# Kernel optimization log

Hardware: AMD Instinct MI355X
Metric: run time of the kernel (lower is better)

The kernel has to match this reference:

```python
import jax, jax.numpy as jnp
import numpy as np
import math

B, S, D, H = 2, 2048, 1024, 16
DH = D // H  # dim_per_head = 64


def setup_inputs() -> dict:
    key = jax.random.key(0)
    ks = jax.random.split(key, 12)
    s = 1.0 / math.sqrt(D)
    return {
        "key": jax.random.normal(ks[0], (B, S, D), jnp.float32),
        "value": jax.random.normal(ks[1], (B, S, D), jnp.float32),
        "query": jax.random.normal(ks[2], (B, S, D), jnp.float32),
        "mask": jax.random.randint(ks[3], (B, S, S), 0, 2).astype(bool),
        "Wq": jax.random.normal(ks[4], (D, D), jnp.float32) * s,
        "bq": jnp.zeros((D,), jnp.float32),
        "Wk": jax.random.normal(ks[5], (D, D), jnp.float32) * s,
        "bk": jnp.zeros((D,), jnp.float32),
        "Wv": jax.random.normal(ks[6], (D, D), jnp.float32) * s,
        "bv": jnp.zeros((D,), jnp.float32),
        "Wo": jax.random.normal(ks[7], (D, D), jnp.float32) * s,
        "bo": jnp.zeros((D,), jnp.float32),
    }


def _shape(x):
    # [B, S, D] -> [B, H, S, DH]
    return x.reshape(B, -1, H, DH).transpose(0, 2, 1, 3)


def reference(key, value, query, mask, Wq, bq, Wk, bk, Wv, bv, Wo, bo):
    q = _shape(query @ Wq.T + bq)  # [B,H,Sq,DH]
    k = _shape(key @ Wk.T + bk)    # [B,H,Sk,DH]
    v = _shape(value @ Wv.T + bv)  # [B,H,Sk,DH]
    q = q / jnp.sqrt(jnp.asarray(DH, q.dtype))
    scores = jnp.einsum("bhqd,bhkd->bhqk", q, k)
    scores = jnp.where(mask[:, None, :, :], jnp.asarray(-1e18, scores.dtype), scores)
    attn = jax.nn.softmax(scores, axis=-1)
    # dropout is identity in eval/deterministic reference
    ctx = jnp.einsum("bhqk,bhkd->bhqd", attn, v)
    ctx = ctx.transpose(0, 2, 1, 3).reshape(B, -1, D)  # unshape
    return ctx @ Wo.T + bo
```

## Files before the change

### kernel.cpp

```cpp
#include <hip/hip_runtime.h>
#include <math.h>


constexpr int Bc  = 2;
constexpr int Sc  = 2048;
constexpr int Dc  = 1024;
constexpr int Hc  = 16;
constexpr int DHc = 64;
constexpr int BSc = Bc * Sc;

constexpr float LOG2E = 1.4426950408889634f;

typedef __bf16 bf16x8 __attribute__((ext_vector_type(8)));
typedef __bf16 bf16x4 __attribute__((ext_vector_type(4)));
typedef __bf16 bf16x2 __attribute__((ext_vector_type(2)));
typedef float  f32x4  __attribute__((ext_vector_type(4)));
typedef float  f32x16 __attribute__((ext_vector_type(16)));
typedef unsigned uint32x2 __attribute__((ext_vector_type(2)));
typedef unsigned uint32x4 __attribute__((ext_vector_type(4)));

#define GLDS16(gp, lp) __builtin_amdgcn_global_load_lds( \
    (const __attribute__((address_space(1))) void*)(gp), \
    (__attribute__((address_space(3))) void*)(lp), 16, 0, 0)

__global__ __launch_bounds__(256)
void wsplit(const float* __restrict__ W0, const float* __restrict__ W1,
            const float* __restrict__ W2, const float* __restrict__ W3,
            __bf16* __restrict__ out)
{
    const float* src[4] = {W0, W1, W2, W3};
    const int z = blockIdx.y;
    const size_t idx = ((size_t)blockIdx.x * 256 + threadIdx.x) * 4;
    const float4 v = *(const float4*)&src[z][idx];
    bf16x4 o;
    o[0] = (__bf16)v.x; o[1] = (__bf16)v.y; o[2] = (__bf16)v.z; o[3] = (__bf16)v.w;
    *(bf16x4*)&out[(size_t)z * Dc * Dc + idx] = o;
}

__global__ __launch_bounds__(256)
void acast(const float* __restrict__ A0, const float* __restrict__ A1,
           const float* __restrict__ A2, __bf16* __restrict__ out)
{
    const float* src[3] = {A0, A1, A2};
    const int z = blockIdx.y;
    const size_t idx = ((size_t)blockIdx.x * 256 + threadIdx.x) * 8;
    const float4 a = *(const float4*)&src[z][idx];
    const float4 b = *(const float4*)&src[z][idx + 4];
    bf16x8 o;
    o[0] = (__bf16)a.x; o[1] = (__bf16)a.y; o[2] = (__bf16)a.z; o[3] = (__bf16)a.w;
    o[4] = (__bf16)b.x; o[5] = (__bf16)b.y; o[6] = (__bf16)b.z; o[7] = (__bf16)b.w;
    *(bf16x8*)&out[(size_t)z * BSc * Dc + idx] = o;
}

__device__ __forceinline__ void sweep128bb(const __bf16* __restrict__ A,
                                           const __bf16* __restrict__ Wh,
                                           char* AsB, char* WsB,
                                           int gm0, int gn0, f32x4 acc[4][4])
{
    const int tid  = threadIdx.x;
    const int w    = tid >> 6;
    const int lane = tid & 63;
    const int cc   = lane & 15;
    const int g    = lane >> 4;
    const int wm   = (w & 1) * 64;
    const int wn   = (w >> 1) * 64;

    int wrow[4], wchk[4];
#pragma unroll
    for (int r = 0; r < 4; ++r) {
        const int L = r * 256 + tid;
        wrow[r] = L >> 3;
        wchk[r] = (L & 7) ^ (wrow[r] & 7);
    }

#pragma unroll
    for (int r = 0; r < 4; ++r) {
        GLDS16(Wh + (size_t)(gn0 + wrow[r]) * Dc + wchk[r] * 8,
               WsB + (r * 256 + tid) * 16);
        GLDS16(A + (size_t)(gm0 + wrow[r]) * Dc + wchk[r] * 8,
               AsB + (r * 256 + tid) * 16);
    }

    for (int it = 0; it < Dc / 64; ++it) {
        const char* As = AsB + (it & 1) * 16384;
        const char* Ws = WsB + (it & 1) * 16384;
        __syncthreads();

        if (it + 1 < Dc / 64) {
            const int kn = (it + 1) * 64;
            char* Wn = WsB + ((it + 1) & 1) * 16384;
            char* An = AsB + ((it + 1) & 1) * 16384;
#pragma unroll
            for (int r = 0; r < 4; ++r) {
                GLDS16(Wh + (size_t)(gn0 + wrow[r]) * Dc + kn + wchk[r] * 8,
                       Wn + (r * 256 + tid) * 16);
                GLDS16(A + (size_t)(gm0 + wrow[r]) * Dc + kn + wchk[r] * 8,
                       An + (r * 256 + tid) * 16);
            }
        }

        __builtin_amdgcn_s_setprio(1);
#pragma unroll
        for (int kk = 0; kk < 2; ++kk) {
            const int cb4 = (kk * 4 + g) << 4;
            bf16x8 af[4], bfr[4];
#pragma unroll
            for (int mt = 0; mt < 4; ++mt) {
                const int row = wm + mt * 16 + cc;
                af[mt] = *(const bf16x8*)(As + row * 128 + (cb4 ^ ((row & 7) << 4)));
            }
#pragma unroll
            for (int nt = 0; nt < 4; ++nt) {
                const int row = wn + nt * 16 + cc;
                bfr[nt] = *(const bf16x8*)(Ws + row * 128 + (cb4 ^ ((row & 7) << 4)));
            }
#pragma unroll
            for (int mt = 0; mt < 4; ++mt)
#pragma unroll
                for (int nt = 0; nt < 4; ++nt)
                    acc[mt][nt] = __builtin_amdgcn_mfma_f32_16x16x32_bf16(
                        af[mt], bfr[nt], acc[mt][nt], 0, 0, 0);
        }
        __builtin_amdgcn_s_setprio(0);
    }
}

__device__ __forceinline__ void sweep64p(const __bf16* __restrict__ Ahi,
                                         const __bf16* __restrict__ Alo,
                                         const __bf16* __restrict__ Wh,
                                         char* WsB, char* AhB, char* AlB,
                                         int gm0, int gn0, f32x4 acc[2][4])
{
    const int tid  = threadIdx.x;
    const int w    = tid >> 6;
    const int lane = tid & 63;
    const int cc   = lane & 15;
    const int g    = lane >> 4;
    const int wm   = (w & 1) * 32;
    const int wn   = (w >> 1) * 64;

    int wrow[4], wchk[4];
#pragma unroll
    for (int r = 0; r < 4; ++r) {
        const int L = r * 256 + tid;
        wrow[r] = L >> 3;
        wchk[r] = (L & 7) ^ (wrow[r] & 7);
    }
    int arow[2], achk[2];
#pragma unroll
    for (int r = 0; r < 2; ++r) {
        const int L = r * 256 + tid;
        arow[r] = L >> 3;
        achk[r] = (L & 7) ^ (arow[r] & 7);
    }

#pragma unroll
    for (int r = 0; r < 4; ++r)
        GLDS16(Wh + (size_t)(gn0 + wrow[r]) * Dc + wchk[r] * 8,
               WsB + (r * 256 + tid) * 16);
#pragma unroll
    for (int r = 0; r < 2; ++r) {
        GLDS16(Ahi + (size_t)(gm0 + arow[r]) * Dc + achk[r] * 8,
               AhB + (r * 256 + tid) * 16);
        GLDS16(Alo + (size_t)(gm0 + arow[r]) * Dc + achk[r] * 8,
               AlB + (r * 256 + tid) * 16);
    }

    for (int it = 0; it < Dc / 64; ++it) {
        const char* Ws = WsB + (it & 1) * 16384;
        const char* Ah = AhB + (it & 1) * 8192;
        const char* Al = AlB + (it & 1) * 8192;
        __syncthreads();

        if (it + 1 < Dc / 64) {
            const int kn = (it + 1) * 64;
            char* Wn = WsB + ((it + 1) & 1) * 16384;
            char* Hn = AhB + ((it + 1) & 1) * 8192;
            char* Ln = AlB + ((it + 1) & 1) * 8192;
#pragma unroll
            for (int r = 0; r < 4; ++r)
                GLDS16(Wh + (size_t)(gn0 + wrow[r]) * Dc + kn + wchk[r] * 8,
                       Wn + (r * 256 + tid) * 16);
#pragma unroll
            for (int r = 0; r < 2; ++r) {
                GLDS16(Ahi + (size_t)(gm0 + arow[r]) * Dc + kn + achk[r] * 8,
                       Hn + (r * 256 + tid) * 16);
                GLDS16(Alo + (size_t)(gm0 + arow[r]) * Dc + kn + achk[r] * 8,
                       Ln + (r * 256 + tid) * 16);
            }
        }

#pragma unroll
        for (int kk = 0; kk < 2; ++kk) {
            const int cb4 = (kk * 4 + g) << 4;
            bf16x8 ahi[2], alo[2], bfr[4];
#pragma unroll
            for (int mt = 0; mt < 2; ++mt) {
                const int row = wm + mt * 16 + cc;
                const int off = row * 128 + (cb4 ^ ((row & 7) << 4));
                ahi[mt] = *(const bf16x8*)(Ah + off);
                alo[mt] = *(const bf16x8*)(Al + off);
            }
#pragma unroll
            for (int nt = 0; nt < 4; ++nt) {
                const int row = wn + nt * 16 + cc;
                bfr[nt] = *(const bf16x8*)(Ws + row * 128 + (cb4 ^ ((row & 7) << 4)));
            }
#pragma unroll
            for (int mt = 0; mt < 2; ++mt)
#pragma unroll
                for (int nt = 0; nt < 4; ++nt) {
                    acc[mt][nt] = __builtin_amdgcn_mfma_f32_16x16x32_bf16(
                        ahi[mt], bfr[nt], acc[mt][nt], 0, 0, 0);
                    acc[mt][nt] = __builtin_amdgcn_mfma_f32_16x16x32_bf16(
                        alo[mt], bfr[nt], acc[mt][nt], 0, 0, 0);
                }
        }
    }
}

__global__ __launch_bounds__(256)
void qkv_mfma(const __bf16* __restrict__ Abf, const __bf16* __restrict__ Whi,
              const float* __restrict__ bq, const float* __restrict__ bk,
              const float* __restrict__ bv,
              __bf16* __restrict__ Qo, __bf16* __restrict__ Ko, __bf16* __restrict__ Vt)
{
    __shared__ __align__(16) char smem[65536];

    const int z = blockIdx.z;
    const float* bias = (z == 0) ? bq : (z == 1) ? bk : bv;
    const float scale = (z == 0) ? 0.125f * LOG2E : 1.0f;
    const __bf16* A   = Abf + (size_t)z * BSc * Dc;
    const __bf16* Wh  = Whi + (size_t)z * Dc * Dc;

    const int gm0 = blockIdx.x * 128;
    const int gn0 = blockIdx.y * 128;

    f32x4 acc[4][4];
#pragma unroll
    for (int mt = 0; mt < 4; ++mt)
#pragma unroll
        for (int nt = 0; nt < 4; ++nt) acc[mt][nt] = {0.f, 0.f, 0.f, 0.f};

    sweep128bb(A, Wh, smem, smem + 32768, gm0, gn0, acc);

    const int tid = threadIdx.x;
    const int w = tid >> 6, lane = tid & 63;
    const int cc = lane & 15, g = lane >> 4;
    const int wm = (w & 1) * 64, wn = (w >> 1) * 64;

    float bias4[4];
#pragma unroll
    for (int nt = 0; nt < 4; ++nt) bias4[nt] = bias[gn0 + wn + nt * 16 + cc];

    if (z == 2) {
#pragma unroll
        for (int mt = 0; mt < 4; ++mt)
#pragma unroll
            for (int nt = 0; nt < 4; ++nt) {
                const int col = gn0 + wn + nt * 16 + cc;
                const int h = col >> 6, dh = col & 63;
                const int row0 = gm0 + wm + mt * 16 + g * 4;
                const int b = row0 >> 11, s0 = row0 & 2047;
                bf16x4 vv;
#pragma unroll
                for (int reg = 0; reg < 4; ++reg)
                    vv[reg] = (__bf16)(acc[mt][nt][reg] + bias4[nt]);
                *(bf16x4*)&Vt[(((size_t)(b * Hc + h)) * DHc + dh) * Sc + s0] = vv;
            }
    } else {
        __bf16* O = (z == 0) ? Qo : Ko;
#pragma unroll
        for (int mt = 0; mt < 4; ++mt)
#pragma unroll
            for (int nt = 0; nt < 4; ++nt) {
                const int col = gn0 + wn + nt * 16 + cc;
                const int h = col >> 6, dh = col & 63;
#pragma unroll
                for (int reg = 0; reg < 4; ++reg) {
                    const int row = gm0 + wm + mt * 16 + g * 4 + reg;
                    const int b = row >> 11, s = row & 2047;
                    O[(((size_t)(b * Hc + h)) * Sc + s) * DHc + dh] =
                        (__bf16)((acc[mt][nt][reg] + bias4[nt]) * scale);
                }
            }
    }
}

__global__ __launch_bounds__(256)
void out_mfma(const __bf16* __restrict__ ctxHi, const __bf16* __restrict__ ctxLo,
              const __bf16* __restrict__ Wohi,
              const float* __restrict__ bo, float* __restrict__ out)
{
    __shared__ __align__(16) char smem[65536];

    const int gm0 = blockIdx.x * 64;
    const int gn0 = blockIdx.y * 128;

    f32x4 acc[2][4];
#pragma unroll
    for (int mt = 0; mt < 2; ++mt)
#pragma unroll
        for (int nt = 0; nt < 4; ++nt) acc[mt][nt] = {0.f, 0.f, 0.f, 0.f};

    sweep64p(ctxHi, ctxLo, Wohi, smem, smem + 32768, smem + 49152, gm0, gn0, acc);

    const int tid = threadIdx.x;
    const int w = tid >> 6, lane = tid & 63;
    const int cc = lane & 15, g = lane >> 4;
    const int wm = (w & 1) * 32, wn = (w >> 1) * 64;

    float bias4[4];
#pragma unroll
    for (int nt = 0; nt < 4; ++nt) bias4[nt] = bo[gn0 + wn + nt * 16 + cc];

#pragma unroll
    for (int mt = 0; mt < 2; ++mt)
#pragma unroll
        for (int nt = 0; nt < 4; ++nt) {
            const int col = gn0 + wn + nt * 16 + cc;
#pragma unroll
            for (int reg = 0; reg < 4; ++reg) {
                const int row = gm0 + wm + mt * 16 + g * 4 + reg;
                out[(size_t)row * Dc + col] = acc[mt][nt][reg] + bias4[nt];
            }
        }
}

__global__ __launch_bounds__(256)
void mask_pack(const int* __restrict__ mask, unsigned long long* __restrict__ out)
{
    const int lane = threadIdx.x & 63;
    const size_t waveBase = ((size_t)blockIdx.x * 4 + (threadIdx.x >> 6)) * 256;
    unsigned long long b0 = __ballot(mask[waveBase + lane]        != 0);
    unsigned long long b1 = __ballot(mask[waveBase + 64 + lane]   != 0);
    unsigned long long b2 = __ballot(mask[waveBase + 128 + lane]  != 0);
    unsigned long long b3 = __ballot(mask[waveBase + 192 + lane]  != 0);
    if (lane == 0) {
        unsigned long long* dst = out + (waveBase >> 6);
        dst[0] = b0; dst[1] = b1; dst[2] = b2; dst[3] = b3;
    }
}

__global__ __launch_bounds__(256, 2)
void attn_mfma(const __bf16* __restrict__ Q, const __bf16* __restrict__ K,
               const __bf16* __restrict__ Vt,
               const unsigned long long* __restrict__ mp,
               __bf16* __restrict__ ctxHi, __bf16* __restrict__ ctxLo)
{
    __shared__ __align__(16) char smem[32768];

    const int tid  = threadIdx.x;
    const int w    = tid >> 6;
    const int lane = tid & 63;
    const int c    = lane & 31;
    const int u    = lane >> 5;
    const int bh   = blockIdx.y;
    const int b    = bh >> 4;
    const int h    = bh & 15;
    const int qw   = blockIdx.x * 128 + w * 32;

    const __bf16* Qb  = Q  + (size_t)bh * Sc * DHc;
    const __bf16* Kb  = K  + (size_t)bh * Sc * DHc;
    const __bf16* Vtb = Vt + (size_t)bh * DHc * Sc;

    bf16x8 qa[4];
#pragma unroll
    for (int ch = 0; ch < 4; ++ch)
        qa[ch] = *(const bf16x8*)&Qb[(size_t)(qw + c) * DHc + ch * 16 + u * 8];

    f32x16 o[2];
#pragma unroll
    for (int dt = 0; dt < 2; ++dt)
#pragma unroll
        for (int i = 0; i < 16; ++i) o[dt][i] = 0.f;
    float lp[4] = {0.f, 0.f, 0.f, 0.f};

    const int ci[2] = {tid, 256 + tid};
    int rowi[2], ski[2];
#pragma unroll
    for (int i = 0; i < 2; ++i) {
        rowi[i] = ci[i] >> 3;
        ski[i]  = (ci[i] & 7) ^ (rowi[i] & 7);
    }

#pragma unroll
    for (int i = 0; i < 2; ++i) {
        GLDS16(Kb + (size_t)rowi[i] * DHc + ski[i] * 8,
               smem + ci[i] * 16);
        GLDS16(Vtb + (size_t)rowi[i] * Sc + ski[i] * 8,
               smem + 8192 + ci[i] * 16);
    }

    for (int it = 0; it < 32; ++it) {
        const char* Ks = smem + (it & 1) * 16384;
        const char* Vs = Ks + 8192;

        __syncthreads();

        if (it + 1 < 32) {
            char* Kn = smem + ((it + 1) & 1) * 16384;
            const int kn = (it + 1) * 64;
#pragma unroll
            for (int i = 0; i < 2; ++i) {
                GLDS16(Kb + (size_t)(kn + rowi[i]) * DHc + ski[i] * 8,
                       Kn + ci[i] * 16);
                GLDS16(Vtb + (size_t)rowi[i] * Sc + kn + ski[i] * 8,
                       Kn + 8192 + ci[i] * 16);
            }
        }

        const unsigned long long mw =
            mp[((size_t)(b * Sc + qw + c) << 5) + it];

        f32x16 sc[2];
        __builtin_amdgcn_s_setprio(1);
#pragma unroll
        for (int nt = 0; nt < 2; ++nt) {
            f32x16 z;
#pragma unroll
            for (int i = 0; i < 16; ++i) z[i] = -24.f;
#pragma unroll
            for (int ch = 0; ch < 4; ++ch) {
                const int row = nt * 32 + c;
                const bf16x8 kb = *(const bf16x8*)
                    (Ks + row * 128 + ((ch * 32 + u * 16) ^ ((row & 7) << 4)));
                z = __builtin_amdgcn_mfma_f32_32x32x16_bf16(kb, qa[ch], z, 0, 0, 0);
            }
            sc[nt] = z;
        }
        __builtin_amdgcn_s_setprio(0);

        unsigned pk[2][4][2];
#pragma unroll
        for (int nt = 0; nt < 2; ++nt)
#pragma unroll
            for (int rr = 0; rr < 4; ++rr) {
                const unsigned nib =
                    (unsigned)(mw >> (nt * 32 + rr * 8 + u * 4)) & 0xFu;
                float pv[4];
#pragma unroll
                for (int r = 0; r < 4; ++r) {
                    float p = __builtin_amdgcn_exp2f(sc[nt][rr * 4 + r]);
                    p = (nib & (1u << r)) ? 0.f : p;
                    lp[rr] += p;
                    pv[r] = p;
                }
                bf16x2 t0; t0[0] = (__bf16)pv[0]; t0[1] = (__bf16)pv[1];
                bf16x2 t1; t1[0] = (__bf16)pv[2]; t1[1] = (__bf16)pv[3];
                pk[nt][rr][0] = __builtin_bit_cast(unsigned, t0);
                pk[nt][rr][1] = __builtin_bit_cast(unsigned, t1);
            }

        bf16x8 pa[4];
#pragma unroll
        for (int kc = 0; kc < 4; ++kc) {
            const int nt = kc >> 1;
            const int r0 = (kc & 1) * 2;
            uint32x2 s0 = __builtin_amdgcn_permlane32_swap(
                pk[nt][r0][0], pk[nt][r0 + 1][0], false, false);
            uint32x2 s1 = __builtin_amdgcn_permlane32_swap(
                pk[nt][r0][1], pk[nt][r0 + 1][1], false, false);
            uint32x4 wds;
            wds[0] = s0[0]; wds[1] = s1[0]; wds[2] = s0[1]; wds[3] = s1[1];
            pa[kc] = __builtin_bit_cast(bf16x8, wds);
        }

        __builtin_amdgcn_s_setprio(1);
#pragma unroll
        for (int dt = 0; dt < 2; ++dt)
#pragma unroll
            for (int kc = 0; kc < 4; ++kc) {
                const int row = dt * 32 + c;
                const bf16x8 vb = *(const bf16x8*)
                    (Vs + row * 128 + ((kc * 32 + u * 16) ^ ((row & 7) << 4)));
                o[dt] = __builtin_amdgcn_mfma_f32_32x32x16_bf16(pa[kc], vb, o[dt], 0, 0, 0);
            }
        __builtin_amdgcn_s_setprio(0);
    }

    float lsum = (lp[0] + lp[1]) + (lp[2] + lp[3]);
    lsum += __shfl_xor(lsum, 32);
    const float linv = 1.0f / lsum;

    float inv[16];
#pragma unroll
    for (int i = 0; i < 16; ++i)
        inv[i] = __shfl(linv, (i & 3) + 8 * (i >> 2) + 4 * u);

#pragma unroll
    for (int dt = 0; dt < 2; ++dt)
#pragma unroll
        for (int i = 0; i < 16; ++i) {
            const int q = qw + (i & 3) + 8 * (i >> 2) + 4 * u;
            const size_t idx = ((size_t)b * Sc + q) * Dc + h * 64 + dt * 32 + c;
            const float v = o[dt][i] * inv[i];
            const __bf16 hi = (__bf16)v;
            ctxHi[idx] = hi;
            ctxLo[idx] = (__bf16)(v - (float)hi);
        }
}

extern "C" void kernel_launch(void* const* d_in, const int* in_sizes, int n_in,
                              void* d_out, int out_size, void* d_ws, size_t ws_size,
                              hipStream_t stream)
{
    const float* key   = (const float*)d_in[0];
    const float* value = (const float*)d_in[1];
    const float* query = (const float*)d_in[2];
    const int*   mask  = (const int*)  d_in[3];
    const float* Wq    = (const float*)d_in[4];
    const float* bq    = (const float*)d_in[5];
    const float* Wk    = (const float*)d_in[6];
    const float* bk    = (const float*)d_in[7];
    const float* Wv    = (const float*)d_in[8];
    const float* bv    = (const float*)d_in[9];
    const float* Wo    = (const float*)d_in[10];
    const float* bo    = (const float*)d_in[11];
    float* out = (float*)d_out;

    char* wsb = (char*)d_ws;
    __bf16* Qbf  = (__bf16*)(wsb);
    __bf16* Kbf  = (__bf16*)(wsb + ((size_t)8  << 20));
    __bf16* Vt   = (__bf16*)(wsb + ((size_t)16 << 20));
    unsigned long long* mpk = (unsigned long long*)(wsb + ((size_t)32 << 20));
    __bf16* Whi  = (__bf16*)(wsb + ((size_t)33 << 20));
    __bf16* ctxHi = (__bf16*)(wsb + ((size_t)41 << 20));
    __bf16* ctxLo = (__bf16*)(wsb + ((size_t)49 << 20));
    __bf16* Abf  = (__bf16*)(wsb + ((size_t)57 << 20));

    dim3 gws(Dc * Dc / (256 * 4), 4);
    wsplit<<<gws, 256, 0, stream>>>(Wq, Wk, Wv, Wo, Whi);

    dim3 gac(BSc * Dc / (256 * 8), 3);
    acast<<<gac, 256, 0, stream>>>(query, key, value, Abf);

    dim3 gqkv(BSc / 128, Dc / 128, 3);
    qkv_mfma<<<gqkv, 256, 0, stream>>>(Abf, Whi, bq, bk, bv, Qbf, Kbf, Vt);

    const int mask_n = Bc * Sc * Sc;
    mask_pack<<<mask_n / 1024, 256, 0, stream>>>(mask, mpk);

    dim3 gattn(Sc / 128, Bc * Hc);
    attn_mfma<<<gattn, 256, 0, stream>>>(Qbf, Kbf, Vt, mpk, ctxHi, ctxLo);

    dim3 gout(BSc / 64, Dc / 128);
    out_mfma<<<gout, 256, 0, stream>>>(ctxHi, ctxLo, Whi + (size_t)3 * Dc * Dc,
                                       bo, out);
}
```

Measured before the change: 251.1 us.

## Interleave ctx hi/lo split into K dimension and duplicate Wo for a single GEMM

The attention kernel now writes the hi and lo bf16 parts of the context interleaved into one buffer with K=2048. Wo is cast with each element duplicated, so the output projection becomes a standard bf16 GEMM through the shared 128x128 sweep, templated on K. This removes the dedicated hi/lo sweep and its separate A streams and allows larger 128-row tiles. In exchange the weight buffer and GEMM K length double, and the grid has half as many blocks.

```diff
diff --git a/kernel.cpp b/kernel.cpp
--- a/kernel.cpp
+++ b/kernel.cpp
@@ -26,15 +26,24 @@
 __global__ __launch_bounds__(256)
 void wsplit(const float* __restrict__ W0, const float* __restrict__ W1,
             const float* __restrict__ W2, const float* __restrict__ W3,
-            __bf16* __restrict__ out)
+            __bf16* __restrict__ out, __bf16* __restrict__ out2)
 {
     const float* src[4] = {W0, W1, W2, W3};
     const int z = blockIdx.y;
     const size_t idx = ((size_t)blockIdx.x * 256 + threadIdx.x) * 4;
     const float4 v = *(const float4*)&src[z][idx];
-    bf16x4 o;
-    o[0] = (__bf16)v.x; o[1] = (__bf16)v.y; o[2] = (__bf16)v.z; o[3] = (__bf16)v.w;
-    *(bf16x4*)&out[(size_t)z * Dc * Dc + idx] = o;
+    if (z == 3) {
+        bf16x8 o;
+        o[0] = (__bf16)v.x; o[1] = (__bf16)v.x;
+        o[2] = (__bf16)v.y; o[3] = (__bf16)v.y;
+        o[4] = (__bf16)v.z; o[5] = (__bf16)v.z;
+        o[6] = (__bf16)v.w; o[7] = (__bf16)v.w;
+        *(bf16x8*)&out2[idx * 2] = o;
+    } else {
+        bf16x4 o;
+        o[0] = (__bf16)v.x; o[1] = (__bf16)v.y; o[2] = (__bf16)v.z; o[3] = (__bf16)v.w;
+        *(bf16x4*)&out[(size_t)z * Dc * Dc + idx] = o;
+    }
 }
 
 __global__ __launch_bounds__(256)
@@ -52,6 +61,7 @@
     *(bf16x8*)&out[(size_t)z * BSc * Dc + idx] = o;
 }
 
+template<int KD>
 __device__ __forceinline__ void sweep128bb(const __bf16* __restrict__ A,
                                            const __bf16* __restrict__ Wh,
                                            char* AsB, char* WsB,
@@ -75,26 +85,26 @@
 
 #pragma unroll
     for (int r = 0; r < 4; ++r) {
-        GLDS16(Wh + (size_t)(gn0 + wrow[r]) * Dc + wchk[r] * 8,
+        GLDS16(Wh + (size_t)(gn0 + wrow[r]) * KD + wchk[r] * 8,
                WsB + (r * 256 + tid) * 16);
-        GLDS16(A + (size_t)(gm0 + wrow[r]) * Dc + wchk[r] * 8,
+        GLDS16(A + (size_t)(gm0 + wrow[r]) * KD + wchk[r] * 8,
                AsB + (r * 256 + tid) * 16);
     }
 
-    for (int it = 0; it < Dc / 64; ++it) {
+    for (int it = 0; it < KD / 64; ++it) {
         const char* As = AsB + (it & 1) * 16384;
         const char* Ws = WsB + (it & 1) * 16384;
         __syncthreads();
 
-        if (it + 1 < Dc / 64) {
+        if (it + 1 < KD / 64) {
             const int kn = (it + 1) * 64;
             char* Wn = WsB + ((it + 1) & 1) * 16384;
             char* An = AsB + ((it + 1) & 1) * 16384;
 #pragma unroll
             for (int r = 0; r < 4; ++r) {
-                GLDS16(Wh + (size_t)(gn0 + wrow[r]) * Dc + kn + wchk[r] * 8,
+                GLDS16(Wh + (size_t)(gn0 + wrow[r]) * KD + kn + wchk[r] * 8,
                        Wn + (r * 256 + tid) * 16);
-                GLDS16(A + (size_t)(gm0 + wrow[r]) * Dc + kn + wchk[r] * 8,
+                GLDS16(A + (size_t)(gm0 + wrow[r]) * KD + kn + wchk[r] * 8,
                        An + (r * 256 + tid) * 16);
             }
         }
@@ -122,100 +132,6 @@
                         af[mt], bfr[nt], acc[mt][nt], 0, 0, 0);
         }
         __builtin_amdgcn_s_setprio(0);
-    }
-}
-
-__device__ __forceinline__ void sweep64p(const __bf16* __restrict__ Ahi,
-                                         const __bf16* __restrict__ Alo,
-                                         const __bf16* __restrict__ Wh,
-                                         char* WsB, char* AhB, char* AlB,
-                                         int gm0, int gn0, f32x4 acc[2][4])
-{
-    const int tid  = threadIdx.x;
-    const int w    = tid >> 6;
-    const int lane = tid & 63;
-    const int cc   = lane & 15;
-    const int g    = lane >> 4;
-    const int wm   = (w & 1) * 32;
-    const int wn   = (w >> 1) * 64;
-
-    int wrow[4], wchk[4];
-#pragma unroll
-    for (int r = 0; r < 4; ++r) {
-        const int L = r * 256 + tid;
-        wrow[r] = L >> 3;
-        wchk[r] = (L & 7) ^ (wrow[r] & 7);
-    }
-    int arow[2], achk[2];
-#pragma unroll
-    for (int r = 0; r < 2; ++r) {
-        const int L = r * 256 + tid;
-        arow[r] = L >> 3;
-        achk[r] = (L & 7) ^ (arow[r] & 7);
-    }
-
-#pragma unroll
-    for (int r = 0; r < 4; ++r)
-        GLDS16(Wh + (size_t)(gn0 + wrow[r]) * Dc + wchk[r] * 8,
-               WsB + (r * 256 + tid) * 16);
-#pragma unroll
-    for (int r = 0; r < 2; ++r) {
-        GLDS16(Ahi + (size_t)(gm0 + arow[r]) * Dc + achk[r] * 8,
-               AhB + (r * 256 + tid) * 16);
-        GLDS16(Alo + (size_t)(gm0 + arow[r]) * Dc + achk[r] * 8,
-               AlB + (r * 256 + tid) * 16);
-    }
-
-    for (int it = 0; it < Dc / 64; ++it) {
-        const char* Ws = WsB + (it & 1) * 16384;
-        const char* Ah = AhB + (it & 1) * 8192;
-        const char* Al = AlB + (it & 1) * 8192;
-        __syncthreads();
-
-        if (it + 1 < Dc / 64) {
-            const int kn = (it + 1) * 64;
-            char* Wn = WsB + ((it + 1) & 1) * 16384;
-            char* Hn = AhB + ((it + 1) & 1) * 8192;
-            char* Ln = AlB + ((it + 1) & 1) * 8192;
-#pragma unroll
-            for (int r = 0; r < 4; ++r)
-                GLDS16(Wh + (size_t)(gn0 + wrow[r]) * Dc + kn + wchk[r] * 8,
-                       Wn + (r * 256 + tid) * 16);
-#pragma unroll
-            for (int r = 0; r < 2; ++r) {
-                GLDS16(Ahi + (size_t)(gm0 + arow[r]) * Dc + kn + achk[r] * 8,
-                       Hn + (r * 256 + tid) * 16);
-                GLDS16(Alo + (size_t)(gm0 + arow[r]) * Dc + kn + achk[r] * 8,
-                       Ln + (r * 256 + tid) * 16);
-            }
-        }
-
-#pragma unroll
-        for (int kk = 0; kk < 2; ++kk) {
-            const int cb4 = (kk * 4 + g) << 4;
-            bf16x8 ahi[2], alo[2], bfr[4];
-#pragma unroll
-            for (int mt = 0; mt < 2; ++mt) {
-                const int row = wm + mt * 16 + cc;
-                const int off = row * 128 + (cb4 ^ ((row & 7) << 4));
-                ahi[mt] = *(const bf16x8*)(Ah + off);
-                alo[mt] = *(const bf16x8*)(Al + off);
-            }
-#pragma unroll
-            for (int nt = 0; nt < 4; ++nt) {
-                const int row = wn + nt * 16 + cc;
-                bfr[nt] = *(const bf16x8*)(Ws + row * 128 + (cb4 ^ ((row & 7) << 4)));
-            }
-#pragma unroll
-            for (int mt = 0; mt < 2; ++mt)
-#pragma unroll
-                for (int nt = 0; nt < 4; ++nt) {
-                    acc[mt][nt] = __builtin_amdgcn_mfma_f32_16x16x32_bf16(
-                        ahi[mt], bfr[nt], acc[mt][nt], 0, 0, 0);
-                    acc[mt][nt] = __builtin_amdgcn_mfma_f32_16x16x32_bf16(
-                        alo[mt], bfr[nt], acc[mt][nt], 0, 0, 0);
-                }
-        }
     }
 }
 
@@ -242,7 +158,7 @@
 #pragma unroll
         for (int nt = 0; nt < 4; ++nt) acc[mt][nt] = {0.f, 0.f, 0.f, 0.f};
 
-    sweep128bb(A, Wh, smem, smem + 32768, gm0, gn0, acc);
+    sweep128bb<Dc>(A, Wh, smem, smem + 32768, gm0, gn0, acc);
 
     const int tid = threadIdx.x;
     const int w = tid >> 6, lane = tid & 63;
@@ -288,34 +204,33 @@
 }
 
 __global__ __launch_bounds__(256)
-void out_mfma(const __bf16* __restrict__ ctxHi, const __bf16* __restrict__ ctxLo,
-              const __bf16* __restrict__ Wohi,
+void out_mfma(const __bf16* __restrict__ ctx2, const __bf16* __restrict__ Wo2,
               const float* __restrict__ bo, float* __restrict__ out)
 {
     __shared__ __align__(16) char smem[65536];
 
-    const int gm0 = blockIdx.x * 64;
+    const int gm0 = blockIdx.x * 128;
     const int gn0 = blockIdx.y * 128;
 
-    f32x4 acc[2][4];
-#pragma unroll
-    for (int mt = 0; mt < 2; ++mt)
+    f32x4 acc[4][4];
+#pragma unroll
+    for (int mt = 0; mt < 4; ++mt)
 #pragma unroll
         for (int nt = 0; nt < 4; ++nt) acc[mt][nt] = {0.f, 0.f, 0.f, 0.f};
 
-    sweep64p(ctxHi, ctxLo, Wohi, smem, smem + 32768, smem + 49152, gm0, gn0, acc);
+    sweep128bb<2 * Dc>(ctx2, Wo2, smem, smem + 32768, gm0, gn0, acc);
 
     const int tid = threadIdx.x;
     const int w = tid >> 6, lane = tid & 63;
     const int cc = lane & 15, g = lane >> 4;
-    const int wm = (w & 1) * 32, wn = (w >> 1) * 64;
+    const int wm = (w & 1) * 64, wn = (w >> 1) * 64;
 
     float bias4[4];
 #pragma unroll
     for (int nt = 0; nt < 4; ++nt) bias4[nt] = bo[gn0 + wn + nt * 16 + cc];
 
 #pragma unroll
-    for (int mt = 0; mt < 2; ++mt)
+    for (int mt = 0; mt < 4; ++mt)
 #pragma unroll
         for (int nt = 0; nt < 4; ++nt) {
             const int col = gn0 + wn + nt * 16 + cc;
@@ -346,7 +261,7 @@
 void attn_mfma(const __bf16* __restrict__ Q, const __bf16* __restrict__ K,
                const __bf16* __restrict__ Vt,
                const unsigned long long* __restrict__ mp,
-               __bf16* __restrict__ ctxHi, __bf16* __restrict__ ctxLo)
+               __bf16* __restrict__ ctx2)
 {
     __shared__ __align__(16) char smem[32768];
 
@@ -493,11 +408,13 @@
 #pragma unroll
         for (int i = 0; i < 16; ++i) {
             const int q = qw + (i & 3) + 8 * (i >> 2) + 4 * u;
-            const size_t idx = ((size_t)b * Sc + q) * Dc + h * 64 + dt * 32 + c;
+            const int col = h * 64 + dt * 32 + c;
             const float v = o[dt][i] * inv[i];
             const __bf16 hi = (__bf16)v;
-            ctxHi[idx] = hi;
-            ctxLo[idx] = (__bf16)(v - (float)hi);
+            bf16x2 hv;
+            hv[0] = hi;
+            hv[1] = (__bf16)(v - (float)hi);
+            *(bf16x2*)&ctx2[(((size_t)b * Sc + q) * Dc + col) * 2] = hv;
         }
 }
 
@@ -523,14 +440,14 @@
     __bf16* Qbf  = (__bf16*)(wsb);
     __bf16* Kbf  = (__bf16*)(wsb + ((size_t)8  << 20));
     __bf16* Vt   = (__bf16*)(wsb + ((size_t)16 << 20));
-    unsigned long long* mpk = (unsigned long long*)(wsb + ((size_t)32 << 20));
-    __bf16* Whi  = (__bf16*)(wsb + ((size_t)33 << 20));
-    __bf16* ctxHi = (__bf16*)(wsb + ((size_t)41 << 20));
-    __bf16* ctxLo = (__bf16*)(wsb + ((size_t)49 << 20));
-    __bf16* Abf  = (__bf16*)(wsb + ((size_t)57 << 20));
+    unsigned long long* mpk = (unsigned long long*)(wsb + ((size_t)24 << 20));
+    __bf16* Whi  = (__bf16*)(wsb + ((size_t)25 << 20));
+    __bf16* Wo2  = (__bf16*)(wsb + ((size_t)31 << 20));
+    __bf16* ctx2 = (__bf16*)(wsb + ((size_t)35 << 20));
+    __bf16* Abf  = (__bf16*)(wsb + ((size_t)51 << 20));
 
     dim3 gws(Dc * Dc / (256 * 4), 4);
-    wsplit<<<gws, 256, 0, stream>>>(Wq, Wk, Wv, Wo, Whi);
+    wsplit<<<gws, 256, 0, stream>>>(Wq, Wk, Wv, Wo, Whi, Wo2);
 
     dim3 gac(BSc * Dc / (256 * 8), 3);
     acast<<<gac, 256, 0, stream>>>(query, key, value, Abf);
@@ -542,9 +459,8 @@
     mask_pack<<<mask_n / 1024, 256, 0, stream>>>(mask, mpk);
 
     dim3 gattn(Sc / 128, Bc * Hc);
-    attn_mfma<<<gattn, 256, 0, stream>>>(Qbf, Kbf, Vt, mpk, ctxHi, ctxLo);
-
-    dim3 gout(BSc / 64, Dc / 128);
-    out_mfma<<<gout, 256, 0, stream>>>(ctxHi, ctxLo, Whi + (size_t)3 * Dc * Dc,
-                                       bo, out);
-}
+    attn_mfma<<<gattn, 256, 0, stream>>>(Qbf, Kbf, Vt, mpk, ctx2);
+
+    dim3 gout(BSc / 128, Dc / 128);
+    out_mfma<<<gout, 256, 0, stream>>>(ctx2, Wo2, bo, out);
+}
```

Result: slower. 268.1 us (+6.8%).
